# Optimization experiments

Measured on AMD Instinct MI355X. Metric: run time of the kernel, lower is better.

## Reference

```python
import jax, jax.numpy as jnp
import numpy as np

NUM_LABELS_I = 28  # 7 entity types * 4 (B/I/E/S)
NUM_LABELS = 31    # + O, EOS, BOS
INDEX_O, INDEX_EOS, INDEX_BOS = 28, 29, 30
NEG = -10000.0


def _make_trans(rng):
    # replicate ChainCRF4NestedNER.reset_parameters() structural masking
    bs = np.arange(0, NUM_LABELS_I, 4)
    is_ = bs + 1
    es = bs + 2
    ss = bs + 3
    t = (rng.standard_normal((NUM_LABELS, NUM_LABELS)) * 0.1).astype(np.float32)
    for i in bs:
        t[i, :i + 1] = NEG; t[i, i + 3:] = NEG
    for i in is_:
        t[i, :i] = NEG; t[i, i + 2:] = NEG
    for i in np.concatenate([es, ss, [INDEX_O]]):
        t[i, is_] = NEG; t[i, es] = NEG; t[i, INDEX_BOS] = NEG
    t[INDEX_EOS, :INDEX_EOS] = NEG; t[INDEX_EOS, INDEX_BOS] = NEG
    t[INDEX_BOS, is_] = NEG; t[INDEX_BOS, es] = NEG; t[INDEX_BOS, INDEX_BOS] = NEG
    return jnp.asarray(t)


def setup_inputs() -> dict:
    B, T, D = 64, 512, 768
    key = jax.random.key(0)
    k1, k2, k3 = jax.random.split(key, 3)
    inp = jax.random.normal(k1, (B, T, D), dtype=jnp.float32)
    target = jax.random.randint(k2, (B, T), 0, 29, dtype=jnp.int64)  # real labels + O only
    mask = jnp.ones((B, T), dtype=jnp.float32)
    state_w = jax.random.normal(k3, (NUM_LABELS, D), dtype=jnp.float32) * 0.02
    state_b = jnp.concatenate([jnp.zeros(INDEX_EOS, jnp.float32),
                               jnp.full(NUM_LABELS - INDEX_EOS, NEG, jnp.float32)])
    trans = _make_trans(np.random.default_rng(0))
    return {"input": inp, "target": target, "mask": mask,
            "state_w": state_w, "state_b": state_b, "trans": trans}


def reference(input, target, mask, state_w, state_b, trans):
    B, T, _ = input.shape
    # state scores [B, T, L]
    out_s = jnp.einsum('btd,ld->btl', input, state_w) + state_b
    out_s = out_s.at[:, :, INDEX_EOS].add((mask == 0).astype(out_s.dtype) * 20000.0)
    # energy [B, T, L, L]: trans[prev, curr] + state[curr]
    energy = trans[None, None, :, :] + out_s[:, :, None, :]
    # forward algorithm (logsumexp semiring) as a scan over time
    energy_t = jnp.moveaxis(energy, 1, 0)  # [T, B, L, L]
    part0 = energy_t[0, :, INDEX_BOS, :]   # [B, L]

    def step(part, e_t):
        new = jax.nn.logsumexp(e_t + part[:, :, None], axis=1)
        return new, None

    partition, _ = jax.lax.scan(step, part0, energy_t[1:])
    # gold-path energy: sum_t energy[b, t, prev_label, label]
    prev = jnp.concatenate([jnp.full((B, 1), INDEX_BOS, dtype=target.dtype),
                            target[:, :-1]], axis=1)
    bi = jnp.arange(B)[:, None]
    ti = jnp.arange(T)[None, :]
    tgt_energy = energy[bi, ti, prev, target].sum(axis=1)
    loss = jax.nn.logsumexp(trans[:, INDEX_EOS][None, :] + partition, axis=1) - tgt_energy
    return loss, energy
```

## Files before the change

kernel.cpp:

```cpp
#include <hip/hip_runtime.h>

typedef float f32x4  __attribute__((ext_vector_type(4)));
typedef float f32x16 __attribute__((ext_vector_type(16)));
typedef short s16x8  __attribute__((ext_vector_type(8)));

constexpr int NL  = 31;
constexpr int BB  = 64;
constexpr int TT  = 512;
constexpr int DD  = 768;
constexpr int RTOT = BB * TT;
constexpr int IDX_EOS = 29;
constexpr int IDX_BOS = 30;
constexpr float LOG2E = 1.4426950408889634f;
constexpr float LN2F  = 0.6931471805599453f;

union Frag8 { unsigned u[4]; s16x8 s; };

__device__ inline unsigned pk2(float a, float b) {
  unsigned ua = __float_as_uint(a), ub = __float_as_uint(b);
  ua = (ua + 0x7fffu + ((ua >> 16) & 1u)) >> 16;
  ub = (ub + 0x7fffu + ((ub >> 16) & 1u)) >> 16;
  return ua | (ub << 16);
}
__device__ inline unsigned short bf16r(float a) {
  unsigned ua = __float_as_uint(a);
  return (unsigned short)((ua + 0x7fffu + ((ua >> 16) & 1u)) >> 16);
}

__device__ inline float bfly_max32(float v) {
#define STEPM(K) { float o = __int_as_float(__builtin_amdgcn_ds_swizzle(__float_as_int(v), ((K) << 10) | 0x1f)); v = fmaxf(v, o); }
  STEPM(1) STEPM(2) STEPM(4) STEPM(8) STEPM(16)
#undef STEPM
  return v;
}
__device__ inline float bfly_sum32(float v) {
#define STEPS(K) { float o = __int_as_float(__builtin_amdgcn_ds_swizzle(__float_as_int(v), ((K) << 10) | 0x1f)); v = v + o; }
  STEPS(1) STEPS(2) STEPS(4) STEPS(8) STEPS(16)
#undef STEPS
  return v;
}

__device__ inline void repack(const float E[16], int h, Frag8& B1, Frag8& B2) {
  unsigned o1a = pk2(E[4 * h], E[4 * h + 1]), o1b = pk2(E[4 * h + 2], E[4 * h + 3]);
  unsigned o2a = pk2(E[8 + 4 * h], E[8 + 4 * h + 1]), o2b = pk2(E[8 + 4 * h + 2], E[8 + 4 * h + 3]);
  int hb = 4 * (1 - h);
  unsigned s1a = pk2(E[hb], E[hb + 1]),         s1b = pk2(E[hb + 2], E[hb + 3]);
  unsigned s2a = pk2(E[8 + hb], E[8 + hb + 1]), s2b = pk2(E[8 + hb + 2], E[8 + hb + 3]);
  unsigned r1a = __shfl_xor((int)s1a, 32), r1b = __shfl_xor((int)s1b, 32);
  unsigned r2a = __shfl_xor((int)s2a, 32), r2b = __shfl_xor((int)s2b, 32);
  if (h == 0) {
    B1.u[0] = o1a; B1.u[1] = o1b; B1.u[2] = r1a; B1.u[3] = r1b;
    B2.u[0] = o2a; B2.u[1] = o2b; B2.u[2] = r2a; B2.u[3] = r2b;
  } else {
    B1.u[0] = r1a; B1.u[1] = r1b; B1.u[2] = o1a; B1.u[3] = o1b;
    B2.u[0] = r2a; B2.u[1] = r2b; B2.u[2] = o2a; B2.u[3] = o2b;
  }
}

__device__ inline void renorm16(float E[16], float& Sacc) {
  float m = E[0];
#pragma unroll
  for (int r = 1; r < 16; ++r) m = fmaxf(m, E[r]);
  m = bfly_max32(m);
  m = fmaxf(m, __shfl_xor(m, 32));
  float lg = truncf(log2f(m));
  Sacc += lg;
  float sc = exp2f(-lg);
#pragma unroll
  for (int r = 0; r < 16; ++r) E[r] *= sc;
}

__device__ inline void load_A16(const unsigned short* M, int l, int h, Frag8& A1, Frag8& A2) {
  A1.s = *(const s16x8*)(M + l * 32 + 8 * h);
  A2.s = *(const s16x8*)(M + l * 32 + 16 + 8 * h);
}
__device__ inline void load_B16(const unsigned short* M, int l, int h, Frag8& B1, Frag8& B2) {
#pragma unroll
  for (int m = 0; m < 4; ++m) {
    int k = 8 * h + 2 * m;
    unsigned lo0 = M[k * 32 + l],        hi0 = M[(k + 1) * 32 + l];
    unsigned lo1 = M[(k + 16) * 32 + l], hi1 = M[(k + 17) * 32 + l];
    B1.u[m] = lo0 | (hi0 << 16);
    B2.u[m] = lo1 | (hi1 << 16);
  }
}

__global__ void k_prep(const float* __restrict__ sw, unsigned short* __restrict__ Bw) {
  for (int i = blockIdx.x * 256 + threadIdx.x; i < 32 * DD; i += 8 * 256)
    Bw[i] = (i < NL * DD) ? bf16r(sw[i]) : (unsigned short)0;
}

__global__ __launch_bounds__(256) void k_outs(
    const float* __restrict__ inp, const unsigned short* __restrict__ Bw,
    const float* __restrict__ sb, const float* __restrict__ msk,
    const float* __restrict__ trans, const int* __restrict__ target,
    float* __restrict__ outs, float* __restrict__ energy,
    float* __restrict__ ws_partial)
{
  __shared__ __align__(16) unsigned short As[4][16 * 72];
  __shared__ float tr[961];
  __shared__ float osh[64 * NL];
  int tid = threadIdx.x, wave = tid >> 6, lane = tid & 63;
  int quad = lane >> 4, l15 = lane & 15;
  int r0 = blockIdx.x * 64;
  int rw = r0 + wave * 16;

  for (int idx = tid; idx < 961; idx += 256) tr[idx] = trans[idx];

  int srow = lane >> 2, scol = lane & 3;
  const float* gsrc = inp + (size_t)(rw + srow) * DD + scol * 4;
  unsigned short* asb = As[wave];
  unsigned* dw = (unsigned*)asb;
  int wbase = srow * 36 + scol * 2;

  f32x4 pre[4];
#pragma unroll
  for (int i = 0; i < 4; ++i) pre[i] = *(const f32x4*)(gsrc + i * 16);

  f32x4 acc[2] = {};
  for (int kc = 0; kc < 12; ++kc) {
#pragma unroll
    for (int i = 0; i < 4; ++i) {
      dw[wbase + i * 8]     = pk2(pre[i][0], pre[i][1]);
      dw[wbase + i * 8 + 1] = pk2(pre[i][2], pre[i][3]);
    }
    if (kc < 11) {
      const float* g2 = gsrc + (kc + 1) * 64;
#pragma unroll
      for (int i = 0; i < 4; ++i) pre[i] = *(const f32x4*)(g2 + i * 16);
    }
#pragma unroll
    for (int ks = 0; ks < 2; ++ks) {
      s16x8 af = *(const s16x8*)(asb + l15 * 72 + ks * 32 + quad * 8);
#pragma unroll
      for (int ct = 0; ct < 2; ++ct) {
        s16x8 bf = *(const s16x8*)(Bw + (ct * 16 + l15) * DD + kc * 64 + ks * 32 + quad * 8);
        acc[ct] = __builtin_amdgcn_mfma_f32_16x16x32_bf16(af, bf, acc[ct], 0, 0, 0);
      }
    }
  }
#pragma unroll
  for (int ct = 0; ct < 2; ++ct) {
    int n = ct * 16 + l15;
    if (n >= NL) continue;
    float b = sb[n];
#pragma unroll
    for (int r = 0; r < 4; ++r) {
      int lr = wave * 16 + quad * 4 + r;
      int row = r0 + lr;
      float v = acc[ct][r] + b;
      if (n == IDX_EOS && msk[row] == 0.f) v += 20000.f;
      osh[lr * NL + n] = v;
      outs[(size_t)row * NL + n] = v;
    }
  }
  __syncthreads();

  if (tid < 64) {
    int r = r0 + tid;
    int tg = target[r];
    int prv = ((r & (TT - 1)) == 0) ? IDX_BOS : target[r - 1];
    float cc = tr[prv * NL + tg] + osh[tid * NL + tg];
#pragma unroll
    for (int off = 32; off; off >>= 1) cc += __shfl_down(cc, off);
    if (tid == 0) ws_partial[blockIdx.x] = cc;
  }

  float* dst = energy + (size_t)r0 * 961;
#pragma unroll 4
  for (int it = 0; it < 60; ++it) {
    int v = it * 256 + tid;
    int e = v * 4;
    f32x4 val;
#pragma unroll
    for (int k = 0; k < 4; ++k) {
      unsigned x = e + k;
      unsigned q = __umulhi(x, 4469269u);
      unsigned c = x - q * 961u;
      unsigned j = c - 31u * ((c * 67651u) >> 21);
      val[k] = tr[c] + osh[q * NL + j];
    }
    *(f32x4*)(dst + e) = val;
  }
  if (tid < 16) {
    int e = (15360 + tid) * 4;
    f32x4 val;
#pragma unroll
    for (int k = 0; k < 4; ++k) {
      unsigned x = e + k;
      unsigned q = __umulhi(x, 4469269u);
      unsigned c = x - q * 961u;
      unsigned j = c - 31u * ((c * 67651u) >> 21);
      val[k] = tr[c] + osh[q * NL + j];
    }
    *(f32x4*)(dst + e) = val;
  }
}

__global__ __launch_bounds__(256) void k_seg(
    const float* __restrict__ outs, const float* __restrict__ trans,
    unsigned short* __restrict__ Mq16, float* __restrict__ Sq)
{
  __shared__ float ub4[4][256];
  __shared__ __align__(16) unsigned short Ms[4][1024];
  __shared__ float Ss[4];
  int tid = threadIdx.x, wave = tid >> 6, lane = tid & 63;
  int l = lane & 31, h = lane >> 5;
  int unit = blockIdx.x * 4 + wave;
  int b = unit >> 6, c = unit & 63;
  int t0 = 1 + c * 8;
  int n = (c == 63) ? 7 : 8;

  float* ub = ub4[wave];
#pragma unroll
  for (int it = 0; it < 4; ++it) {
    int idx = lane + it * 64;
    int row = idx >> 5, col = idx & 31;
    float v = 0.f;
    if (col < NL && row < n)
      v = exp2f(LOG2E * outs[((size_t)b * TT + t0 + row) * NL + col]);
    ub[idx] = v;
  }

  Frag8 A1, A2, B1, B2;
#pragma unroll
  for (int m = 0; m < 4; ++m) {
    int k0 = 8 * h + 2 * m, k1 = k0 + 1;
    float a0 = (k0 < NL && l < NL) ? exp2f(LOG2E * trans[k0 * NL + l]) : 0.f;
    float a1 = (k1 < NL && l < NL) ? exp2f(LOG2E * trans[k1 * NL + l]) : 0.f;
    A1.u[m] = pk2(a0, a1);
    int k2 = 16 + k0, k3 = 16 + k1;
    float a2 = (k2 < NL && l < NL) ? exp2f(LOG2E * trans[k2 * NL + l]) : 0.f;
    float a3 = (k3 < NL && l < NL) ? exp2f(LOG2E * trans[k3 * NL + l]) : 0.f;
    A2.u[m] = pk2(a2, a3);
    B1.u[m] = ((k0 == l) ? 0x3f80u : 0u) | (((k1 == l) ? 0x3f80u : 0u) << 16);
    B2.u[m] = ((k2 == l) ? 0x3f80u : 0u) | (((k3 == l) ? 0x3f80u : 0u) << 16);
  }

  float E[16];
  for (int s = 0; s < n; ++s) {
    const float* us = ub + s * 32 + 4 * h;
    f32x4 u0 = *(const f32x4*)(us);
    f32x4 u1 = *(const f32x4*)(us + 8);
    f32x4 u2 = *(const f32x4*)(us + 16);
    f32x4 u3 = *(const f32x4*)(us + 24);
    f32x16 D = {};
    D = __builtin_amdgcn_mfma_f32_32x32x16_bf16(A1.s, B1.s, D, 0, 0, 0);
    D = __builtin_amdgcn_mfma_f32_32x32x16_bf16(A2.s, B2.s, D, 0, 0, 0);
#pragma unroll
    for (int jj = 0; jj < 4; ++jj) {
      E[jj]      = D[jj]      * u0[jj];
      E[4 + jj]  = D[4 + jj]  * u1[jj];
      E[8 + jj]  = D[8 + jj]  * u2[jj];
      E[12 + jj] = D[12 + jj] * u3[jj];
    }
    if (s + 1 < n) repack(E, h, B1, B2);
  }
  float S = 0.f;
  renorm16(E, S);
  unsigned short* mo = Ms[wave];
#pragma unroll
  for (int r = 0; r < 16; ++r) {
    int row = (r & 3) + 8 * (r >> 2) + 4 * h;
    mo[row * 32 + l] = bf16r(E[r]);
  }
  if (lane == 0) Ss[wave] = S;
  __syncthreads();

  if (wave == 0) {
    load_B16(Ms[0], l, h, B1, B2);
    float Sx = Ss[0] + Ss[1] + Ss[2] + Ss[3];
    float E2[16];
#pragma unroll
    for (int i = 1; i < 4; ++i) {
      load_A16(Ms[i], l, h, A1, A2);
      f32x16 D = {};
      D = __builtin_amdgcn_mfma_f32_32x32x16_bf16(A1.s, B1.s, D, 0, 0, 0);
      D = __builtin_amdgcn_mfma_f32_32x32x16_bf16(A2.s, B2.s, D, 0, 0, 0);
#pragma unroll
      for (int r = 0; r < 16; ++r) E2[r] = D[r];
      if (i < 3) repack(E2, h, B1, B2);
    }
    renorm16(E2, Sx);
    unsigned short* qo = Mq16 + (size_t)blockIdx.x * 1024;
#pragma unroll
    for (int r = 0; r < 16; ++r) {
      int row = (r & 3) + 8 * (r >> 2) + 4 * h;
      qo[row * 32 + l] = bf16r(E2[r]);
    }
    if (lane == 0) Sq[blockIdx.x] = Sx;
  }
}

__global__ __launch_bounds__(256) void k_tree2(
    const float* __restrict__ outs, const float* __restrict__ trans,
    const unsigned short* __restrict__ Mq16, const float* __restrict__ Sq,
    const float* __restrict__ ws_partial, float* __restrict__ loss)
{
  int tid = threadIdx.x, wave = tid >> 6, lane = tid & 63;
  int l = lane & 31, h = lane >> 5;
  int b = blockIdx.x * 4 + wave;
  const unsigned short* base = Mq16 + (size_t)b * 16384;
  Frag8 A1, A2, B1, B2;
  load_B16(base, l, h, B1, B2);
  float S = 0.f;
#pragma unroll
  for (int q = 0; q < 16; ++q) S += Sq[b * 16 + q];
  float E[16];
  for (int i = 1; i < 16; ++i) {
    load_A16(base + i * 1024, l, h, A1, A2);
    f32x16 D = {};
    D = __builtin_amdgcn_mfma_f32_32x32x16_bf16(A1.s, B1.s, D, 0, 0, 0);
    D = __builtin_amdgcn_mfma_f32_32x32x16_bf16(A2.s, B2.s, D, 0, 0, 0);
#pragma unroll
    for (int r = 0; r < 16; ++r) E[r] = D[r];
    if ((i & 3) == 3) renorm16(E, S);
    if (i < 15) repack(E, h, B1, B2);
  }
  float p0 = (l < NL) ? exp2f(LOG2E * (trans[IDX_BOS * NL + l] + outs[(size_t)b * TT * NL + l])) : 0.f;
  float sum_h = 0.f;
#pragma unroll
  for (int r = 0; r < 16; ++r) {
    float s = bfly_sum32(E[r] * p0);
    int row = (r & 3) + 8 * (r >> 2) + 4 * h;
    float We = (row < NL) ? exp2f(LOG2E * trans[row * NL + IDX_EOS]) : 0.f;
    sum_h += s * We;
  }
  float tot = sum_h + __shfl_xor(sum_h, 32);
  if (lane == 0) {
    float wst = 0.f;
#pragma unroll
    for (int i = 0; i < 8; ++i) wst += ws_partial[b * 8 + i];
    loss[b] = LN2F * (S + log2f(tot)) - wst;
  }
}

extern "C" void kernel_launch(void* const* d_in, const int* in_sizes, int n_in,
                              void* d_out, int out_size, void* d_ws, size_t ws_size,
                              hipStream_t stream) {
  const float* inp   = (const float*)d_in[0];
  const int*   tgt   = (const int*)d_in[1];
  const float* msk   = (const float*)d_in[2];
  const float* sw    = (const float*)d_in[3];
  const float* sb    = (const float*)d_in[4];
  const float* trans = (const float*)d_in[5];

  float* out    = (float*)d_out;
  float* loss   = out;
  float* energy = out + BB;

  float* outs        = (float*)d_ws;
  float* Sq          = outs + (size_t)RTOT * NL;
  float* ws_partial  = Sq + 1024;
  unsigned short* Mq16 = (unsigned short*)(ws_partial + 512);
  unsigned short* Bw   = Mq16 + (size_t)1024 * 1024;

  k_prep<<<8, 256, 0, stream>>>(sw, Bw);
  k_outs<<<RTOT / 64, 256, 0, stream>>>(inp, Bw, sb, msk, trans, tgt, outs, energy, ws_partial);
  k_seg<<<1024, 256, 0, stream>>>(outs, trans, Mq16, Sq);
  k_tree2<<<16, 256, 0, stream>>>(outs, trans, Mq16, Sq, ws_partial, loss);
}
```

Measured before the change: 305.5 us.

## Fuse GEMM, segment scan and tree reduction into one cooperative kernel

Merges the three phase kernels into a single cooperative kernel with 512 blocks, using grid-wide syncs between phases. The shared-memory layout is a union reused across phases. The final per-batch chain product changes from a sequential 16-step loop to a parallel binary tree across four waves in shared memory. This removes two kernel launches and the serial reduction depth, but adds grid-sync overhead and relies on 512 blocks of 256 threads being co-resident.

```diff
diff --git a/kernel.cpp b/kernel.cpp
--- a/kernel.cpp
+++ b/kernel.cpp
@@ -1,4 +1,7 @@
 #include <hip/hip_runtime.h>
+#include <hip/hip_cooperative_groups.h>
+
+namespace cg = cooperative_groups;
 
 typedef float f32x4  __attribute__((ext_vector_type(4)));
 typedef float f32x16 __attribute__((ext_vector_type(16)));
@@ -85,253 +88,300 @@
   }
 }
 
+__device__ inline void tree_node(unsigned short* Tb, float* Ts, int ja, int jb, int l, int h) {
+  Frag8 A1, A2, B1, B2;
+  load_A16(Tb + ja * 1024, l, h, A1, A2);
+  load_B16(Tb + jb * 1024, l, h, B1, B2);
+  f32x16 D = {};
+  D = __builtin_amdgcn_mfma_f32_32x32x16_bf16(A1.s, B1.s, D, 0, 0, 0);
+  D = __builtin_amdgcn_mfma_f32_32x32x16_bf16(A2.s, B2.s, D, 0, 0, 0);
+  float E[16];
+#pragma unroll
+  for (int r = 0; r < 16; ++r) E[r] = D[r];
+  float S = Ts[ja] + Ts[jb];
+  renorm16(E, S);
+#pragma unroll
+  for (int r = 0; r < 16; ++r) {
+    int row = (r & 3) + 8 * (r >> 2) + 4 * h;
+    Tb[jb * 1024 + row * 32 + l] = bf16r(E[r]);
+  }
+  if (l == 0 && h == 0) Ts[jb] = S;
+}
+
 __global__ void k_prep(const float* __restrict__ sw, unsigned short* __restrict__ Bw) {
   for (int i = blockIdx.x * 256 + threadIdx.x; i < 32 * DD; i += 8 * 256)
     Bw[i] = (i < NL * DD) ? bf16r(sw[i]) : (unsigned short)0;
 }
 
-__global__ __launch_bounds__(256) void k_outs(
+__global__ __launch_bounds__(256, 2) void k_fused(
     const float* __restrict__ inp, const unsigned short* __restrict__ Bw,
     const float* __restrict__ sb, const float* __restrict__ msk,
     const float* __restrict__ trans, const int* __restrict__ target,
     float* __restrict__ outs, float* __restrict__ energy,
-    float* __restrict__ ws_partial)
+    float* __restrict__ ws_partial, unsigned short* __restrict__ Mq16,
+    float* __restrict__ Sq, float* __restrict__ loss)
 {
-  __shared__ __align__(16) unsigned short As[4][16 * 72];
-  __shared__ float tr[961];
-  __shared__ float osh[64 * NL];
+  __shared__ __align__(16) union {
+    struct { unsigned short As[4][16 * 72]; float tr[961]; float osh[64 * NL]; } p1;
+    struct { float ub[4][256]; unsigned short Ms[2][4][1024]; float Ss[2][4]; } p2;
+    struct { unsigned short T[16][1024]; float Ts[16]; } p3;
+  } sm;
+
+  cg::grid_group grid = cg::this_grid();
   int tid = threadIdx.x, wave = tid >> 6, lane = tid & 63;
-  int quad = lane >> 4, l15 = lane & 15;
-  int r0 = blockIdx.x * 64;
-  int rw = r0 + wave * 16;
-
-  for (int idx = tid; idx < 961; idx += 256) tr[idx] = trans[idx];
-
-  int srow = lane >> 2, scol = lane & 3;
-  const float* gsrc = inp + (size_t)(rw + srow) * DD + scol * 4;
-  unsigned short* asb = As[wave];
-  unsigned* dw = (unsigned*)asb;
-  int wbase = srow * 36 + scol * 2;
-
-  f32x4 pre[4];
-#pragma unroll
-  for (int i = 0; i < 4; ++i) pre[i] = *(const f32x4*)(gsrc + i * 16);
-
-  f32x4 acc[2] = {};
-  for (int kc = 0; kc < 12; ++kc) {
-#pragma unroll
-    for (int i = 0; i < 4; ++i) {
-      dw[wbase + i * 8]     = pk2(pre[i][0], pre[i][1]);
-      dw[wbase + i * 8 + 1] = pk2(pre[i][2], pre[i][3]);
-    }
-    if (kc < 11) {
-      const float* g2 = gsrc + (kc + 1) * 64;
-#pragma unroll
-      for (int i = 0; i < 4; ++i) pre[i] = *(const f32x4*)(g2 + i * 16);
-    }
-#pragma unroll
-    for (int ks = 0; ks < 2; ++ks) {
-      s16x8 af = *(const s16x8*)(asb + l15 * 72 + ks * 32 + quad * 8);
-#pragma unroll
-      for (int ct = 0; ct < 2; ++ct) {
-        s16x8 bf = *(const s16x8*)(Bw + (ct * 16 + l15) * DD + kc * 64 + ks * 32 + quad * 8);
-        acc[ct] = __builtin_amdgcn_mfma_f32_16x16x32_bf16(af, bf, acc[ct], 0, 0, 0);
-      }
-    }
-  }
-#pragma unroll
-  for (int ct = 0; ct < 2; ++ct) {
-    int n = ct * 16 + l15;
-    if (n >= NL) continue;
-    float b = sb[n];
-#pragma unroll
-    for (int r = 0; r < 4; ++r) {
-      int lr = wave * 16 + quad * 4 + r;
-      int row = r0 + lr;
-      float v = acc[ct][r] + b;
-      if (n == IDX_EOS && msk[row] == 0.f) v += 20000.f;
-      osh[lr * NL + n] = v;
-      outs[(size_t)row * NL + n] = v;
-    }
-  }
-  __syncthreads();
-
-  if (tid < 64) {
-    int r = r0 + tid;
-    int tg = target[r];
-    int prv = ((r & (TT - 1)) == 0) ? IDX_BOS : target[r - 1];
-    float cc = tr[prv * NL + tg] + osh[tid * NL + tg];
-#pragma unroll
-    for (int off = 32; off; off >>= 1) cc += __shfl_down(cc, off);
-    if (tid == 0) ws_partial[blockIdx.x] = cc;
-  }
-
-  float* dst = energy + (size_t)r0 * 961;
+
+  {
+    int quad = lane >> 4, l15 = lane & 15;
+    int r0 = blockIdx.x * 64;
+    int rw = r0 + wave * 16;
+
+    for (int idx = tid; idx < 961; idx += 256) sm.p1.tr[idx] = trans[idx];
+
+    int srow = lane >> 2, scol = lane & 3;
+    const float* gsrc = inp + (size_t)(rw + srow) * DD + scol * 4;
+    unsigned short* asb = sm.p1.As[wave];
+    unsigned* dw = (unsigned*)asb;
+    int wbase = srow * 36 + scol * 2;
+
+    f32x4 pre[4];
+#pragma unroll
+    for (int i = 0; i < 4; ++i) pre[i] = *(const f32x4*)(gsrc + i * 16);
+
+    f32x4 acc[2] = {};
+    for (int kc = 0; kc < 12; ++kc) {
+#pragma unroll
+      for (int i = 0; i < 4; ++i) {
+        dw[wbase + i * 8]     = pk2(pre[i][0], pre[i][1]);
+        dw[wbase + i * 8 + 1] = pk2(pre[i][2], pre[i][3]);
+      }
+      if (kc < 11) {
+        const float* g2 = gsrc + (kc + 1) * 64;
+#pragma unroll
+        for (int i = 0; i < 4; ++i) pre[i] = *(const f32x4*)(g2 + i * 16);
+      }
+#pragma unroll
+      for (int ks = 0; ks < 2; ++ks) {
+        s16x8 af = *(const s16x8*)(asb + l15 * 72 + ks * 32 + quad * 8);
+#pragma unroll
+        for (int ct = 0; ct < 2; ++ct) {
+          s16x8 bf = *(const s16x8*)(Bw + (ct * 16 + l15) * DD + kc * 64 + ks * 32 + quad * 8);
+          acc[ct] = __builtin_amdgcn_mfma_f32_16x16x32_bf16(af, bf, acc[ct], 0, 0, 0);
+        }
+      }
+    }
+#pragma unroll
+    for (int ct = 0; ct < 2; ++ct) {
+      int n = ct * 16 + l15;
+      if (n >= NL) continue;
+      float b = sb[n];
+#pragma unroll
+      for (int r = 0; r < 4; ++r) {
+        int lr = wave * 16 + quad * 4 + r;
+        int row = r0 + lr;
+        float v = acc[ct][r] + b;
+        if (n == IDX_EOS && msk[row] == 0.f) v += 20000.f;
+        sm.p1.osh[lr * NL + n] = v;
+        outs[(size_t)row * NL + n] = v;
+      }
+    }
+    __syncthreads();
+
+    if (tid < 64) {
+      int r = r0 + tid;
+      int tg = target[r];
+      int prv = ((r & (TT - 1)) == 0) ? IDX_BOS : target[r - 1];
+      float cc = sm.p1.tr[prv * NL + tg] + sm.p1.osh[tid * NL + tg];
+#pragma unroll
+      for (int off = 32; off; off >>= 1) cc += __shfl_down(cc, off);
+      if (tid == 0) ws_partial[blockIdx.x] = cc;
+    }
+
+    float* dst = energy + (size_t)r0 * 961;
 #pragma unroll 4
-  for (int it = 0; it < 60; ++it) {
-    int v = it * 256 + tid;
-    int e = v * 4;
-    f32x4 val;
-#pragma unroll
-    for (int k = 0; k < 4; ++k) {
-      unsigned x = e + k;
-      unsigned q = __umulhi(x, 4469269u);
-      unsigned c = x - q * 961u;
-      unsigned j = c - 31u * ((c * 67651u) >> 21);
-      val[k] = tr[c] + osh[q * NL + j];
-    }
-    *(f32x4*)(dst + e) = val;
-  }
-  if (tid < 16) {
-    int e = (15360 + tid) * 4;
-    f32x4 val;
-#pragma unroll
-    for (int k = 0; k < 4; ++k) {
-      unsigned x = e + k;
-      unsigned q = __umulhi(x, 4469269u);
-      unsigned c = x - q * 961u;
-      unsigned j = c - 31u * ((c * 67651u) >> 21);
-      val[k] = tr[c] + osh[q * NL + j];
-    }
-    *(f32x4*)(dst + e) = val;
-  }
-}
-
-__global__ __launch_bounds__(256) void k_seg(
-    const float* __restrict__ outs, const float* __restrict__ trans,
-    unsigned short* __restrict__ Mq16, float* __restrict__ Sq)
-{
-  __shared__ float ub4[4][256];
-  __shared__ __align__(16) unsigned short Ms[4][1024];
-  __shared__ float Ss[4];
-  int tid = threadIdx.x, wave = tid >> 6, lane = tid & 63;
-  int l = lane & 31, h = lane >> 5;
-  int unit = blockIdx.x * 4 + wave;
-  int b = unit >> 6, c = unit & 63;
-  int t0 = 1 + c * 8;
-  int n = (c == 63) ? 7 : 8;
-
-  float* ub = ub4[wave];
-#pragma unroll
-  for (int it = 0; it < 4; ++it) {
-    int idx = lane + it * 64;
-    int row = idx >> 5, col = idx & 31;
-    float v = 0.f;
-    if (col < NL && row < n)
-      v = exp2f(LOG2E * outs[((size_t)b * TT + t0 + row) * NL + col]);
-    ub[idx] = v;
-  }
-
-  Frag8 A1, A2, B1, B2;
-#pragma unroll
-  for (int m = 0; m < 4; ++m) {
-    int k0 = 8 * h + 2 * m, k1 = k0 + 1;
-    float a0 = (k0 < NL && l < NL) ? exp2f(LOG2E * trans[k0 * NL + l]) : 0.f;
-    float a1 = (k1 < NL && l < NL) ? exp2f(LOG2E * trans[k1 * NL + l]) : 0.f;
-    A1.u[m] = pk2(a0, a1);
-    int k2 = 16 + k0, k3 = 16 + k1;
-    float a2 = (k2 < NL && l < NL) ? exp2f(LOG2E * trans[k2 * NL + l]) : 0.f;
-    float a3 = (k3 < NL && l < NL) ? exp2f(LOG2E * trans[k3 * NL + l]) : 0.f;
-    A2.u[m] = pk2(a2, a3);
-    B1.u[m] = ((k0 == l) ? 0x3f80u : 0u) | (((k1 == l) ? 0x3f80u : 0u) << 16);
-    B2.u[m] = ((k2 == l) ? 0x3f80u : 0u) | (((k3 == l) ? 0x3f80u : 0u) << 16);
-  }
-
-  float E[16];
-  for (int s = 0; s < n; ++s) {
-    const float* us = ub + s * 32 + 4 * h;
-    f32x4 u0 = *(const f32x4*)(us);
-    f32x4 u1 = *(const f32x4*)(us + 8);
-    f32x4 u2 = *(const f32x4*)(us + 16);
-    f32x4 u3 = *(const f32x4*)(us + 24);
-    f32x16 D = {};
-    D = __builtin_amdgcn_mfma_f32_32x32x16_bf16(A1.s, B1.s, D, 0, 0, 0);
-    D = __builtin_amdgcn_mfma_f32_32x32x16_bf16(A2.s, B2.s, D, 0, 0, 0);
-#pragma unroll
-    for (int jj = 0; jj < 4; ++jj) {
-      E[jj]      = D[jj]      * u0[jj];
-      E[4 + jj]  = D[4 + jj]  * u1[jj];
-      E[8 + jj]  = D[8 + jj]  * u2[jj];
-      E[12 + jj] = D[12 + jj] * u3[jj];
-    }
-    if (s + 1 < n) repack(E, h, B1, B2);
-  }
-  float S = 0.f;
-  renorm16(E, S);
-  unsigned short* mo = Ms[wave];
-#pragma unroll
-  for (int r = 0; r < 16; ++r) {
-    int row = (r & 3) + 8 * (r >> 2) + 4 * h;
-    mo[row * 32 + l] = bf16r(E[r]);
-  }
-  if (lane == 0) Ss[wave] = S;
-  __syncthreads();
-
-  if (wave == 0) {
-    load_B16(Ms[0], l, h, B1, B2);
-    float Sx = Ss[0] + Ss[1] + Ss[2] + Ss[3];
-    float E2[16];
-#pragma unroll
-    for (int i = 1; i < 4; ++i) {
-      load_A16(Ms[i], l, h, A1, A2);
+    for (int it = 0; it < 60; ++it) {
+      int v = it * 256 + tid;
+      int e = v * 4;
+      f32x4 val;
+#pragma unroll
+      for (int k = 0; k < 4; ++k) {
+        unsigned x = e + k;
+        unsigned q = __umulhi(x, 4469269u);
+        unsigned c = x - q * 961u;
+        unsigned j = c - 31u * ((c * 67651u) >> 21);
+        val[k] = sm.p1.tr[c] + sm.p1.osh[q * NL + j];
+      }
+      *(f32x4*)(dst + e) = val;
+    }
+    if (tid < 16) {
+      int e = (15360 + tid) * 4;
+      f32x4 val;
+#pragma unroll
+      for (int k = 0; k < 4; ++k) {
+        unsigned x = e + k;
+        unsigned q = __umulhi(x, 4469269u);
+        unsigned c = x - q * 961u;
+        unsigned j = c - 31u * ((c * 67651u) >> 21);
+        val[k] = sm.p1.tr[c] + sm.p1.osh[q * NL + j];
+      }
+      *(f32x4*)(dst + e) = val;
+    }
+  }
+
+  __threadfence();
+  grid.sync();
+
+  {
+    int l = lane & 31, h = lane >> 5;
+
+    Frag8 At1, At2;
+#pragma unroll
+    for (int m = 0; m < 4; ++m) {
+      int k0 = 8 * h + 2 * m, k1 = k0 + 1;
+      float a0 = (k0 < NL && l < NL) ? exp2f(LOG2E * trans[k0 * NL + l]) : 0.f;
+      float a1 = (k1 < NL && l < NL) ? exp2f(LOG2E * trans[k1 * NL + l]) : 0.f;
+      At1.u[m] = pk2(a0, a1);
+      int k2 = 16 + k0, k3 = 16 + k1;
+      float a2 = (k2 < NL && l < NL) ? exp2f(LOG2E * trans[k2 * NL + l]) : 0.f;
+      float a3 = (k3 < NL && l < NL) ? exp2f(LOG2E * trans[k3 * NL + l]) : 0.f;
+      At2.u[m] = pk2(a2, a3);
+    }
+
+#pragma unroll
+    for (int rep = 0; rep < 2; ++rep) {
+      int unit = blockIdx.x * 8 + rep * 4 + wave;
+      int b = unit >> 6, c = unit & 63;
+      int t0 = 1 + c * 8;
+      int n = (c == 63) ? 7 : 8;
+
+      float* ub = sm.p2.ub[wave];
+#pragma unroll
+      for (int it = 0; it < 4; ++it) {
+        int idx = lane + it * 64;
+        int row = idx >> 5, col = idx & 31;
+        float v = 0.f;
+        if (col < NL && row < n)
+          v = exp2f(LOG2E * outs[((size_t)b * TT + t0 + row) * NL + col]);
+        ub[idx] = v;
+      }
+
+      Frag8 B1, B2;
+#pragma unroll
+      for (int m = 0; m < 4; ++m) {
+        int k0 = 8 * h + 2 * m, k1 = k0 + 1;
+        int k2 = 16 + k0, k3 = 16 + k1;
+        B1.u[m] = ((k0 == l) ? 0x3f80u : 0u) | (((k1 == l) ? 0x3f80u : 0u) << 16);
+        B2.u[m] = ((k2 == l) ? 0x3f80u : 0u) | (((k3 == l) ? 0x3f80u : 0u) << 16);
+      }
+
+      float E[16];
+      for (int s = 0; s < n; ++s) {
+        const float* us = ub + s * 32 + 4 * h;
+        f32x4 u0 = *(const f32x4*)(us);
+        f32x4 u1 = *(const f32x4*)(us + 8);
+        f32x4 u2 = *(const f32x4*)(us + 16);
+        f32x4 u3 = *(const f32x4*)(us + 24);
+        f32x16 D = {};
+        D = __builtin_amdgcn_mfma_f32_32x32x16_bf16(At1.s, B1.s, D, 0, 0, 0);
+        D = __builtin_amdgcn_mfma_f32_32x32x16_bf16(At2.s, B2.s, D, 0, 0, 0);
+#pragma unroll
+        for (int jj = 0; jj < 4; ++jj) {
+          E[jj]      = D[jj]      * u0[jj];
+          E[4 + jj]  = D[4 + jj]  * u1[jj];
+          E[8 + jj]  = D[8 + jj]  * u2[jj];
+          E[12 + jj] = D[12 + jj] * u3[jj];
+        }
+        if (s + 1 < n) repack(E, h, B1, B2);
+      }
+      float S = 0.f;
+      renorm16(E, S);
+      unsigned short* mo = sm.p2.Ms[rep][wave];
+#pragma unroll
+      for (int r = 0; r < 16; ++r) {
+        int row = (r & 3) + 8 * (r >> 2) + 4 * h;
+        mo[row * 32 + l] = bf16r(E[r]);
+      }
+      if (lane == 0) sm.p2.Ss[rep][wave] = S;
+    }
+    __syncthreads();
+
+    if (wave < 2) {
+      Frag8 A1, A2, B1, B2;
+      load_B16(sm.p2.Ms[wave][0], l, h, B1, B2);
+      float Sx = sm.p2.Ss[wave][0] + sm.p2.Ss[wave][1] + sm.p2.Ss[wave][2] + sm.p2.Ss[wave][3];
+      float E2[16];
+#pragma unroll
+      for (int i = 1; i < 4; ++i) {
+        load_A16(sm.p2.Ms[wave][i], l, h, A1, A2);
+        f32x16 D = {};
+        D = __builtin_amdgcn_mfma_f32_32x32x16_bf16(A1.s, B1.s, D, 0, 0, 0);
+        D = __builtin_amdgcn_mfma_f32_32x32x16_bf16(A2.s, B2.s, D, 0, 0, 0);
+#pragma unroll
+        for (int r = 0; r < 16; ++r) E2[r] = D[r];
+        if (i < 3) repack(E2, h, B1, B2);
+      }
+      renorm16(E2, Sx);
+      int qg = blockIdx.x * 2 + wave;
+      unsigned short* qo = Mq16 + (size_t)qg * 1024;
+#pragma unroll
+      for (int r = 0; r < 16; ++r) {
+        int row = (r & 3) + 8 * (r >> 2) + 4 * h;
+        qo[row * 32 + l] = bf16r(E2[r]);
+      }
+      if (lane == 0) Sq[qg] = Sx;
+    }
+  }
+
+  __threadfence();
+  grid.sync();
+
+  if (blockIdx.x < BB) {
+    int bb = blockIdx.x;
+    int l = lane & 31, h = lane >> 5;
+    unsigned* Td = (unsigned*)sm.p3.T;
+    const unsigned* src = (const unsigned*)(Mq16 + (size_t)bb * 16384);
+    for (int idx = tid; idx < 8192; idx += 256) Td[idx] = src[idx];
+    if (tid < 16) sm.p3.Ts[tid] = Sq[bb * 16 + tid];
+    __syncthreads();
+
+    unsigned short* T = sm.p3.T[0];
+    float* Ts = sm.p3.Ts;
+
+    tree_node(T, Ts, 2 * wave + 1, 2 * wave, l, h);
+    tree_node(T, Ts, 2 * (wave + 4) + 1, 2 * (wave + 4), l, h);
+    __syncthreads();
+    tree_node(T, Ts, 4 * wave + 2, 4 * wave, l, h);
+    __syncthreads();
+    if (wave < 2) tree_node(T, Ts, 8 * wave + 4, 8 * wave, l, h);
+    __syncthreads();
+    if (wave == 0) {
+      Frag8 A1, A2, B1, B2;
+      load_A16(T + 8 * 1024, l, h, A1, A2);
+      load_B16(T, l, h, B1, B2);
       f32x16 D = {};
       D = __builtin_amdgcn_mfma_f32_32x32x16_bf16(A1.s, B1.s, D, 0, 0, 0);
       D = __builtin_amdgcn_mfma_f32_32x32x16_bf16(A2.s, B2.s, D, 0, 0, 0);
-#pragma unroll
-      for (int r = 0; r < 16; ++r) E2[r] = D[r];
-      if (i < 3) repack(E2, h, B1, B2);
-    }
-    renorm16(E2, Sx);
-    unsigned short* qo = Mq16 + (size_t)blockIdx.x * 1024;
-#pragma unroll
-    for (int r = 0; r < 16; ++r) {
-      int row = (r & 3) + 8 * (r >> 2) + 4 * h;
-      qo[row * 32 + l] = bf16r(E2[r]);
-    }
-    if (lane == 0) Sq[blockIdx.x] = Sx;
-  }
-}
-
-__global__ __launch_bounds__(256) void k_tree2(
-    const float* __restrict__ outs, const float* __restrict__ trans,
-    const unsigned short* __restrict__ Mq16, const float* __restrict__ Sq,
-    const float* __restrict__ ws_partial, float* __restrict__ loss)
-{
-  int tid = threadIdx.x, wave = tid >> 6, lane = tid & 63;
-  int l = lane & 31, h = lane >> 5;
-  int b = blockIdx.x * 4 + wave;
-  const unsigned short* base = Mq16 + (size_t)b * 16384;
-  Frag8 A1, A2, B1, B2;
-  load_B16(base, l, h, B1, B2);
-  float S = 0.f;
-#pragma unroll
-  for (int q = 0; q < 16; ++q) S += Sq[b * 16 + q];
-  float E[16];
-  for (int i = 1; i < 16; ++i) {
-    load_A16(base + i * 1024, l, h, A1, A2);
-    f32x16 D = {};
-    D = __builtin_amdgcn_mfma_f32_32x32x16_bf16(A1.s, B1.s, D, 0, 0, 0);
-    D = __builtin_amdgcn_mfma_f32_32x32x16_bf16(A2.s, B2.s, D, 0, 0, 0);
-#pragma unroll
-    for (int r = 0; r < 16; ++r) E[r] = D[r];
-    if ((i & 3) == 3) renorm16(E, S);
-    if (i < 15) repack(E, h, B1, B2);
-  }
-  float p0 = (l < NL) ? exp2f(LOG2E * (trans[IDX_BOS * NL + l] + outs[(size_t)b * TT * NL + l])) : 0.f;
-  float sum_h = 0.f;
-#pragma unroll
-  for (int r = 0; r < 16; ++r) {
-    float s = bfly_sum32(E[r] * p0);
-    int row = (r & 3) + 8 * (r >> 2) + 4 * h;
-    float We = (row < NL) ? exp2f(LOG2E * trans[row * NL + IDX_EOS]) : 0.f;
-    sum_h += s * We;
-  }
-  float tot = sum_h + __shfl_xor(sum_h, 32);
-  if (lane == 0) {
-    float wst = 0.f;
-#pragma unroll
-    for (int i = 0; i < 8; ++i) wst += ws_partial[b * 8 + i];
-    loss[b] = LN2F * (S + log2f(tot)) - wst;
+      float E[16];
+#pragma unroll
+      for (int r = 0; r < 16; ++r) E[r] = D[r];
+      float S = Ts[0] + Ts[8];
+
+      float p0 = (l < NL) ? exp2f(LOG2E * (trans[IDX_BOS * NL + l] + outs[(size_t)bb * TT * NL + l])) : 0.f;
+      float sum_h = 0.f;
+#pragma unroll
+      for (int r = 0; r < 16; ++r) {
+        float s = bfly_sum32(E[r] * p0);
+        int row = (r & 3) + 8 * (r >> 2) + 4 * h;
+        float We = (row < NL) ? exp2f(LOG2E * trans[row * NL + IDX_EOS]) : 0.f;
+        sum_h += s * We;
+      }
+      float tot = sum_h + __shfl_xor(sum_h, 32);
+      if (lane == 0) {
+        float wst = 0.f;
+#pragma unroll
+        for (int i = 0; i < 8; ++i) wst += ws_partial[bb * 8 + i];
+        loss[bb] = LN2F * (S + log2f(tot)) - wst;
+      }
+    }
   }
 }
 
@@ -356,7 +406,11 @@
   unsigned short* Bw   = Mq16 + (size_t)1024 * 1024;
 
   k_prep<<<8, 256, 0, stream>>>(sw, Bw);
-  k_outs<<<RTOT / 64, 256, 0, stream>>>(inp, Bw, sb, msk, trans, tgt, outs, energy, ws_partial);
-  k_seg<<<1024, 256, 0, stream>>>(outs, trans, Mq16, Sq);
-  k_tree2<<<16, 256, 0, stream>>>(outs, trans, Mq16, Sq, ws_partial, loss);
-}
+
+  const unsigned short* Bw_c = Bw;
+  void* args[] = {
+    (void*)&inp, (void*)&Bw_c, (void*)&sb, (void*)&msk, (void*)&trans, (void*)&tgt,
+    (void*)&outs, (void*)&energy, (void*)&ws_partial, (void*)&Mq16, (void*)&Sq, (void*)&loss
+  };
+  hipLaunchCooperativeKernel((void*)k_fused, dim3(512), dim3(256), args, 0, stream);
+}
```

Measured after the change: 501.2 us. 64.1% more time.
